# Kernel tuning notes

Hardware: AMD Instinct MI355X
Metric: run time of the kernel (lower is better)

Reference implementation:

```python
import jax, jax.numpy as jnp
import numpy as np

VOCAB, D = 50000, 300
B, LC = 64, 32
T, LT = 256, 64
N_SENTS = 5


def setup_inputs() -> dict:
    key = jax.random.key(0)
    k1, k2, k3 = jax.random.split(key, 3)
    claim = jax.random.randint(k1, (B, LC), 0, VOCAB)
    targets = jax.random.randint(k2, (B, T, LT), 0, VOCAB)
    embeddings = jax.random.normal(k3, (VOCAB, D), dtype=jnp.float32)
    return {"claim": claim, "targets": targets, "embeddings": embeddings, "n": N_SENTS}


def reference(claim, targets, embeddings, n):
    # Embedding lookups (frozen table)
    c = embeddings[claim]          # [B, Lc, d]
    t = embeddings[targets]        # [B, T, Lt, d]
    # batch_U = claim[:,None] @ targets^T  -> [B, T, Lc, Lt]
    U = jnp.einsum('bcd,btld->btcl', c, t)
    # softmax over target tokens (axis=3), max over claim tokens (axis=2)
    sm = jax.nn.softmax(U, axis=3)
    scores = jnp.max(sm, axis=2)           # [B, T, Lt]
    target_scores = jnp.sum(scores, axis=2)  # [B, T]
    # per-batch top-n target sentences (sorted order; torch used sorted=False,
    # the selected set is identical)
    _, idx = jax.lax.top_k(target_scores, n)  # [B, n]
    top = jnp.take_along_axis(U, idx[:, :, None, None], axis=1)  # [B, n, Lc, Lt]
    # L2-normalize over last axis (torch dim=2 of the [n, Lc, Lt] slice)
    norm = jnp.sqrt(jnp.sum(top * top, axis=3, keepdims=True))
    return top / norm
```

## Files before the change

kernel.cpp:

```cpp
#include <hip/hip_runtime.h>

#define VOCAB 50000
#define D     300
#define B_    64
#define LC    32
#define T_    256
#define LT    64
#define NSEL  5
#define NCAND 16

#define A_U4   2560
#define A_HALF 20480
#define TROW   320

typedef _Float16 half8_t __attribute__((ext_vector_type(8)));
typedef float    f32x4   __attribute__((ext_vector_type(4)));


__global__ __launch_bounds__(256) void k_prep(const int* __restrict__ claim,
                                              const float* __restrict__ emb,
                                              _Float16* __restrict__ tab,
                                              _Float16* __restrict__ wsA,
                                              int tableBlocks) {
    int wave = threadIdx.x >> 6, lane = threadIdx.x & 63;
    if ((int)blockIdx.x < tableBlocks) {
#pragma unroll
        for (int it = 0; it < 8; ++it) {
            int r = blockIdx.x * 32 + it * 4 + wave;
            if (r < VOCAB) {
                const float* src = emb + (size_t)r * D;
                _Float16* d = tab + (size_t)r * TROW;
#pragma unroll
                for (int i = 0; i < 5; ++i) {
                    int k = lane + i * 64;
                    d[k] = (k < D) ? (_Float16)src[k] : (_Float16)0.0f;
                }
            }
        }
    } else {
#pragma unroll
        for (int it = 0; it < 8; ++it) {
            int row = (blockIdx.x - tableBlocks) * 32 + it * 4 + wave;
            int b = row >> 5, m = row & 31;
            int tok = claim[row];
            const float* src = emb + (size_t)tok * D;
            _Float16* base = wsA + (size_t)b * A_HALF;
#pragma unroll
            for (int i = 0; i < 5; ++i) {
                int k = lane + i * 64;
                float x = (k < D) ? src[k] : 0.0f;
                _Float16 h = (_Float16)x;
                int sp = ((k >> 3) ^ (m & 7));
                int idx = (m * 40 + sp) * 8 + (k & 7);
                base[idx] = h;
                base[10240 + idx] = (_Float16)(x - (float)h);
            }
        }
    }
}

__device__ __forceinline__ void split8(const float4& a, const float4& b,
                                       half8_t& hv, half8_t& lv) {
    float x[8] = {a.x, a.y, a.z, a.w, b.x, b.y, b.z, b.w};
#pragma unroll
    for (int i = 0; i < 8; ++i) {
        _Float16 h = (_Float16)x[i];
        hv[i] = h;
        lv[i] = (_Float16)(x[i] - (float)h);
    }
}

template<int NI>
__device__ __forceinline__ void compute_exact(const uint4* sA,
                                              const float* __restrict__ emb,
                                              const int* __restrict__ trow, int lcol0,
                                              int lane, f32x4 acc[2][NI]) {
    int ln = lane & 15, quad = lane >> 4;
#pragma unroll
    for (int mi = 0; mi < 2; ++mi)
#pragma unroll
        for (int ni = 0; ni < NI; ++ni) acc[mi][ni] = (f32x4)0.0f;

    int arow0 = ln * 40;
    int arow1 = (16 + ln) * 40;
    int key = ln & 7;
    int qo = quad * 8;

    const float* bp[NI];
#pragma unroll
    for (int ni = 0; ni < NI; ++ni) {
        int tok = trow[lcol0 + ni * 16 + ln];
        bp[ni] = emb + (size_t)tok * D;
    }
#pragma unroll 1
    for (int ks = 0; ks < 10; ++ks) {
        int kb = ks * 32 + qo;
        int ka = kb > 296 ? 296 : kb;
        int kb4 = kb + 4;
        int kbb = kb4 > 296 ? 296 : kb4;
        float4 b0[NI], b1[NI];
#pragma unroll
        for (int ni = 0; ni < NI; ++ni) {
            b0[ni] = *(const float4*)(bp[ni] + ka);
            b1[ni] = *(const float4*)(bp[ni] + kbb);
        }
        if (kb >= 296) {
            float4 z = make_float4(0.f, 0.f, 0.f, 0.f);
#pragma unroll
            for (int ni = 0; ni < NI; ++ni) {
                if (kb >= 300) b0[ni] = z;
                b1[ni] = z;
            }
        }
        int sp = (ks * 4 + quad) ^ key;
        half8_t ah[2], al[2];
        ah[0] = __builtin_bit_cast(half8_t, sA[arow0 + sp]);
        al[0] = __builtin_bit_cast(half8_t, sA[1280 + arow0 + sp]);
        ah[1] = __builtin_bit_cast(half8_t, sA[arow1 + sp]);
        al[1] = __builtin_bit_cast(half8_t, sA[1280 + arow1 + sp]);
        half8_t bh[NI], bl[NI];
#pragma unroll
        for (int ni = 0; ni < NI; ++ni) split8(b0[ni], b1[ni], bh[ni], bl[ni]);
#pragma unroll
        for (int mi = 0; mi < 2; ++mi)
#pragma unroll
            for (int ni = 0; ni < NI; ++ni) {
                acc[mi][ni] = __builtin_amdgcn_mfma_f32_16x16x32_f16(ah[mi], bh[ni], acc[mi][ni], 0, 0, 0);
                acc[mi][ni] = __builtin_amdgcn_mfma_f32_16x16x32_f16(ah[mi], bl[ni], acc[mi][ni], 0, 0, 0);
                acc[mi][ni] = __builtin_amdgcn_mfma_f32_16x16x32_f16(al[mi], bh[ni], acc[mi][ni], 0, 0, 0);
            }
    }
}

__device__ __forceinline__ void compute_noisy(const uint4* sA,
                                              const _Float16* __restrict__ tab,
                                              const int* __restrict__ trow,
                                              int lane, f32x4 acc[2][4]) {
    int ln = lane & 15, quad = lane >> 4;
#pragma unroll
    for (int mi = 0; mi < 2; ++mi)
#pragma unroll
        for (int ni = 0; ni < 4; ++ni) acc[mi][ni] = (f32x4)0.0f;

    int arow0 = ln * 40;
    int arow1 = (16 + ln) * 40;
    int key = ln & 7;
    int qo = quad * 8;

    const _Float16* rp[4];
#pragma unroll
    for (int ni = 0; ni < 4; ++ni) {
        int tok = trow[ni * 16 + ln];
        rp[ni] = tab + (size_t)tok * TROW;
    }
    half8_t bh[2][4];
#pragma unroll
    for (int ni = 0; ni < 4; ++ni) bh[0][ni] = *(const half8_t*)(rp[ni] + qo);
#pragma unroll
    for (int ks = 0; ks < 10; ++ks) {
        int cur = ks & 1, nxt = cur ^ 1;
        if (ks < 9) {
            int ko = (ks + 1) * 32 + qo;
#pragma unroll
            for (int ni = 0; ni < 4; ++ni)
                bh[nxt][ni] = *(const half8_t*)(rp[ni] + ko);
        }
        int sp = (ks * 4 + quad) ^ key;
        half8_t ah[2], al[2];
        ah[0] = __builtin_bit_cast(half8_t, sA[arow0 + sp]);
        al[0] = __builtin_bit_cast(half8_t, sA[1280 + arow0 + sp]);
        ah[1] = __builtin_bit_cast(half8_t, sA[arow1 + sp]);
        al[1] = __builtin_bit_cast(half8_t, sA[1280 + arow1 + sp]);
#pragma unroll
        for (int mi = 0; mi < 2; ++mi)
#pragma unroll
            for (int ni = 0; ni < 4; ++ni) {
                acc[mi][ni] = __builtin_amdgcn_mfma_f32_16x16x32_f16(ah[mi], bh[cur][ni], acc[mi][ni], 0, 0, 0);
                acc[mi][ni] = __builtin_amdgcn_mfma_f32_16x16x32_f16(al[mi], bh[cur][ni], acc[mi][ni], 0, 0, 0);
            }
    }
}

__device__ __forceinline__ float xmax4(float v) {
    v = fmaxf(v, __shfl_xor(v, 1)); v = fmaxf(v, __shfl_xor(v, 2));
    v = fmaxf(v, __shfl_xor(v, 4)); v = fmaxf(v, __shfl_xor(v, 8));
    return v;
}
__device__ __forceinline__ float xsum4(float v) {
    v += __shfl_xor(v, 1); v += __shfl_xor(v, 2);
    v += __shfl_xor(v, 4); v += __shfl_xor(v, 8);
    return v;
}

__device__ __forceinline__ float score_from_acc(f32x4 acc[2][4]) {
    float score_l[4] = {0.f, 0.f, 0.f, 0.f};
#pragma unroll
    for (int mi = 0; mi < 2; ++mi)
#pragma unroll
        for (int r = 0; r < 4; ++r) {
            float m = fmaxf(fmaxf(acc[mi][0][r], acc[mi][1][r]),
                            fmaxf(acc[mi][2][r], acc[mi][3][r]));
            m = xmax4(m);
            float p[4], s = 0.f;
#pragma unroll
            for (int ni = 0; ni < 4; ++ni) { p[ni] = __expf(acc[mi][ni][r] - m); s += p[ni]; }
            s = xsum4(s);
            float rv = 1.0f / s;
#pragma unroll
            for (int ni = 0; ni < 4; ++ni) score_l[ni] = fmaxf(score_l[ni], p[ni] * rv);
        }
    float tot = 0.f;
#pragma unroll
    for (int ni = 0; ni < 4; ++ni) {
        float v = score_l[ni];
        v = fmaxf(v, __shfl_xor(v, 16));
        v = fmaxf(v, __shfl_xor(v, 32));
        tot += v;
    }
    return xsum4(tot);
}

template<bool FAST>
__global__ __launch_bounds__(256, 4) void k_scores(const int* __restrict__ targets,
                                                   const float* __restrict__ emb,
                                                   const _Float16* __restrict__ tab,
                                                   const _Float16* __restrict__ wsA,
                                                   float* __restrict__ wsScr) {
    __shared__ __align__(16) uint4 sA[A_U4];
    int wg = blockIdx.x;
    int xcd = wg & 7, rest = wg >> 3;
    int b = xcd * 8 + (rest >> 6);
    int tg = rest & 63;
    int tid = threadIdx.x;
    {
        const uint4* src = (const uint4*)(wsA + (size_t)b * A_HALF);
        for (int i = tid; i < A_U4; i += 256) sA[i] = src[i];
    }
    __syncthreads();

    int lane = tid & 63, wave = tid >> 6;
    int t = tg * 4 + wave;
    const int* trow = targets + ((size_t)b * T_ + t) * LT;

    f32x4 acc[2][4];
    if (FAST) compute_noisy(sA, tab, trow, lane, acc);
    else      compute_exact<4>(sA, emb, trow, 0, lane, acc);
    float tot = score_from_acc(acc);
    if (lane == 0) wsScr[b * T_ + t] = tot;
}

__global__ __launch_bounds__(256) void k_sel(const int* __restrict__ targets,
                                             const float* __restrict__ emb,
                                             const _Float16* __restrict__ wsA,
                                             const float* __restrict__ wsScr,
                                             int* __restrict__ wsCand,
                                             float* __restrict__ wsScoreC) {
    __shared__ __align__(16) uint4 sA[A_U4];
    __shared__ int sCand[NCAND];
    int r = blockIdx.x, b = blockIdx.y, tid = threadIdx.x;
    int lane = tid & 63, wave = tid >> 6;
    if (wave) {
        const uint4* src = (const uint4*)(wsA + (size_t)b * A_HALF);
        for (int i = tid - 64; i < A_U4; i += 192) sA[i] = src[i];
    } else {
        float v[4];
#pragma unroll
        for (int i = 0; i < 4; ++i) v[i] = wsScr[b * T_ + lane + 64 * i];
        for (int s = 0; s < NCAND; ++s) {
            float bv = v[0]; int bi = lane;
#pragma unroll
            for (int i = 1; i < 4; ++i) {
                int idx = lane + 64 * i;
                if (v[i] > bv) { bv = v[i]; bi = idx; }
            }
            for (int off = 32; off > 0; off >>= 1) {
                float ov = __shfl_down(bv, off);
                int   oi = __shfl_down(bi, off);
                if (ov > bv || (ov == bv && oi < bi)) { bv = ov; bi = oi; }
            }
            bi = __shfl(bi, 0);
            if (lane == 0) {
                sCand[s] = bi;
                if (r == 0) wsCand[b * NCAND + s] = bi;
            }
            if ((bi & 63) == lane) v[bi >> 6] = -1e30f;
        }
    }
    __syncthreads();

    int c = r * 4 + wave;
    int t = sCand[c];
    const int* trow = targets + ((size_t)b * T_ + t) * LT;
    f32x4 acc[2][4];
    compute_exact<4>(sA, emb, trow, 0, lane, acc);
    float tot = score_from_acc(acc);
    if (lane == 0) wsScoreC[b * NCAND + c] = tot;
}

__global__ __launch_bounds__(256) void k_output(const int* __restrict__ targets,
                                                const float* __restrict__ emb,
                                                const _Float16* __restrict__ wsA,
                                                const int* __restrict__ wsCand,
                                                const float* __restrict__ wsScoreC,
                                                float* __restrict__ out) {
    __shared__ __align__(16) uint4 sA[A_U4];
    __shared__ float sS[LC][4];
    __shared__ int sT;
    int b = blockIdx.y, j = blockIdx.x, tid = threadIdx.x;
    int lane = tid & 63, wave = tid >> 6;
    if (wave) {
        const uint4* src = (const uint4*)(wsA + (size_t)b * A_HALF);
        for (int i = tid - 64; i < A_U4; i += 192) sA[i] = src[i];
    } else if (lane == 0) {
        unsigned used = 0; int sel = 0;
        for (int jj = 0; jj <= j; ++jj) {
            float bs = -1e30f; int bt = 0x7fffffff, bsl = 0;
            for (int s = 0; s < NCAND; ++s) {
                if (used & (1u << s)) continue;
                float sc = wsScoreC[b * NCAND + s];
                int tt = wsCand[b * NCAND + s];
                if (sc > bs || (sc == bs && tt < bt)) { bs = sc; bt = tt; bsl = s; }
            }
            used |= (1u << bsl);
            sel = bt;
        }
        sT = sel;
    }
    __syncthreads();

    int t = sT;
    const int* trow = targets + ((size_t)b * T_ + t) * LT;
    f32x4 acc[2][1];
    compute_exact<1>(sA, emb, trow, wave * 16, lane, acc);

    int ln = lane & 15, quad = lane >> 4;
#pragma unroll
    for (int mi = 0; mi < 2; ++mi)
#pragma unroll
        for (int r = 0; r < 4; ++r) {
            float v = acc[mi][0][r] * acc[mi][0][r];
            v = xsum4(v);
            if (ln == 0) sS[mi * 16 + quad * 4 + r][wave] = v;
        }
    __syncthreads();

    float* obase = out + (size_t)(b * NSEL + j) * (LC * LT);
#pragma unroll
    for (int mi = 0; mi < 2; ++mi)
#pragma unroll
        for (int r = 0; r < 4; ++r) {
            int c = mi * 16 + quad * 4 + r;
            float ss = sS[c][0] + sS[c][1] + sS[c][2] + sS[c][3];
            float rinv = 1.0f / sqrtf(ss);
            obase[c * LT + wave * 16 + ln] = acc[mi][0][r] * rinv;
        }
}

extern "C" void kernel_launch(void* const* d_in, const int* in_sizes, int n_in,
                              void* d_out, int out_size, void* d_ws, size_t ws_size,
                              hipStream_t stream) {
    const int*   claim   = (const int*)d_in[0];
    const int*   targets = (const int*)d_in[1];
    const float* emb     = (const float*)d_in[2];

    const size_t tabBytes = (size_t)VOCAB * TROW * sizeof(_Float16);
    const size_t restBytes = (size_t)B_ * A_HALF * sizeof(_Float16)
                           + (size_t)B_ * T_ * sizeof(float)
                           + (size_t)B_ * NCAND * (sizeof(int) + sizeof(float)) + 256;
    bool fast = ws_size >= tabBytes + restBytes;

    char* p = (char*)d_ws;
    _Float16* tab = nullptr;
    if (fast) { tab = (_Float16*)p; p += tabBytes; }
    _Float16* wsA = (_Float16*)p; p += (size_t)B_ * A_HALF * sizeof(_Float16);
    float* wsScr = (float*)p;     p += (size_t)B_ * T_ * sizeof(float);
    int*   wsCand = (int*)p;      p += (size_t)B_ * NCAND * sizeof(int);
    float* wsScoreC = (float*)p;
    float* out   = (float*)d_out;

    int tableBlocks = fast ? ((VOCAB + 31) / 32) : 0;
    k_prep<<<dim3(tableBlocks + 64), dim3(256), 0, stream>>>(claim, emb, tab, wsA, tableBlocks);
    if (fast) {
        k_scores<true><<<dim3(B_ * 64), dim3(256), 0, stream>>>(targets, emb, tab, wsA, wsScr);
    } else {
        k_scores<false><<<dim3(B_ * 64), dim3(256), 0, stream>>>(targets, emb, tab, wsA, wsScr);
    }
    k_sel<<<dim3(NCAND / 4, B_), dim3(256), 0, stream>>>(targets, emb, wsA, wsScr, wsCand, wsScoreC);
    k_output<<<dim3(NSEL, B_), dim3(256), 0, stream>>>(targets, emb, wsA, wsCand, wsScoreC, out);
}
```

Before: 241.3 us.

## Fuse prep, scoring, selection and output into one cooperative persistent kernel

Replaces the four separate launches (prep, scores, sel, output) with a single cooperative kernel of 1024 blocks that uses grid-wide syncs between the phases. Each block converts table rows in a grid-stride loop, then scores 16 target sentences, and a subset of blocks runs candidate selection and the normalized output. This is meant to remove launch gaps and inter-kernel drain/fill. In exchange, the scoring phase runs with fewer blocks and more serial work per block, and it adds grid-sync costs. If the cooperative launch fails, the code falls back to the old path.

Measured after the change: 725.2 us. +200.6%, slower.

```diff
diff --git a/kernel.cpp b/kernel.cpp
--- a/kernel.cpp
+++ b/kernel.cpp
@@ -1,4 +1,7 @@
 #include <hip/hip_runtime.h>
+#include <hip/hip_cooperative_groups.h>
+
+namespace cg = cooperative_groups;
 
 #define VOCAB 50000
 #define D     300
@@ -17,6 +20,319 @@
 typedef float    f32x4   __attribute__((ext_vector_type(4)));
 
 
+__device__ __forceinline__ void split8(const float4& a, const float4& b,
+                                       half8_t& hv, half8_t& lv) {
+    float x[8] = {a.x, a.y, a.z, a.w, b.x, b.y, b.z, b.w};
+#pragma unroll
+    for (int i = 0; i < 8; ++i) {
+        _Float16 h = (_Float16)x[i];
+        hv[i] = h;
+        lv[i] = (_Float16)(x[i] - (float)h);
+    }
+}
+
+template<int NI>
+__device__ __forceinline__ void compute_exact(const uint4* sA,
+                                              const float* __restrict__ emb,
+                                              const int* __restrict__ trow, int lcol0,
+                                              int lane, f32x4 acc[2][NI]) {
+    int ln = lane & 15, quad = lane >> 4;
+#pragma unroll
+    for (int mi = 0; mi < 2; ++mi)
+#pragma unroll
+        for (int ni = 0; ni < NI; ++ni) acc[mi][ni] = (f32x4)0.0f;
+
+    int arow0 = ln * 40;
+    int arow1 = (16 + ln) * 40;
+    int key = ln & 7;
+    int qo = quad * 8;
+
+    const float* bp[NI];
+#pragma unroll
+    for (int ni = 0; ni < NI; ++ni) {
+        int tok = trow[lcol0 + ni * 16 + ln];
+        bp[ni] = emb + (size_t)tok * D;
+    }
+#pragma unroll 1
+    for (int ks = 0; ks < 10; ++ks) {
+        int kb = ks * 32 + qo;
+        int ka = kb > 296 ? 296 : kb;
+        int kb4 = kb + 4;
+        int kbb = kb4 > 296 ? 296 : kb4;
+        float4 b0[NI], b1[NI];
+#pragma unroll
+        for (int ni = 0; ni < NI; ++ni) {
+            b0[ni] = *(const float4*)(bp[ni] + ka);
+            b1[ni] = *(const float4*)(bp[ni] + kbb);
+        }
+        if (kb >= 296) {
+            float4 z = make_float4(0.f, 0.f, 0.f, 0.f);
+#pragma unroll
+            for (int ni = 0; ni < NI; ++ni) {
+                if (kb >= 300) b0[ni] = z;
+                b1[ni] = z;
+            }
+        }
+        int sp = (ks * 4 + quad) ^ key;
+        half8_t ah[2], al[2];
+        ah[0] = __builtin_bit_cast(half8_t, sA[arow0 + sp]);
+        al[0] = __builtin_bit_cast(half8_t, sA[1280 + arow0 + sp]);
+        ah[1] = __builtin_bit_cast(half8_t, sA[arow1 + sp]);
+        al[1] = __builtin_bit_cast(half8_t, sA[1280 + arow1 + sp]);
+        half8_t bh[NI], bl[NI];
+#pragma unroll
+        for (int ni = 0; ni < NI; ++ni) split8(b0[ni], b1[ni], bh[ni], bl[ni]);
+#pragma unroll
+        for (int mi = 0; mi < 2; ++mi)
+#pragma unroll
+            for (int ni = 0; ni < NI; ++ni) {
+                acc[mi][ni] = __builtin_amdgcn_mfma_f32_16x16x32_f16(ah[mi], bh[ni], acc[mi][ni], 0, 0, 0);
+                acc[mi][ni] = __builtin_amdgcn_mfma_f32_16x16x32_f16(ah[mi], bl[ni], acc[mi][ni], 0, 0, 0);
+                acc[mi][ni] = __builtin_amdgcn_mfma_f32_16x16x32_f16(al[mi], bh[ni], acc[mi][ni], 0, 0, 0);
+            }
+    }
+}
+
+__device__ __forceinline__ void compute_noisy(const uint4* sA,
+                                              const _Float16* __restrict__ tab,
+                                              const int* __restrict__ trow,
+                                              int lane, f32x4 acc[2][4]) {
+    int ln = lane & 15, quad = lane >> 4;
+#pragma unroll
+    for (int mi = 0; mi < 2; ++mi)
+#pragma unroll
+        for (int ni = 0; ni < 4; ++ni) acc[mi][ni] = (f32x4)0.0f;
+
+    int arow0 = ln * 40;
+    int arow1 = (16 + ln) * 40;
+    int key = ln & 7;
+    int qo = quad * 8;
+
+    const _Float16* rp[4];
+#pragma unroll
+    for (int ni = 0; ni < 4; ++ni) {
+        int tok = trow[ni * 16 + ln];
+        rp[ni] = tab + (size_t)tok * TROW;
+    }
+    half8_t bh[2][4];
+#pragma unroll
+    for (int ni = 0; ni < 4; ++ni) bh[0][ni] = *(const half8_t*)(rp[ni] + qo);
+#pragma unroll
+    for (int ks = 0; ks < 10; ++ks) {
+        int cur = ks & 1, nxt = cur ^ 1;
+        if (ks < 9) {
+            int ko = (ks + 1) * 32 + qo;
+#pragma unroll
+            for (int ni = 0; ni < 4; ++ni)
+                bh[nxt][ni] = *(const half8_t*)(rp[ni] + ko);
+        }
+        int sp = (ks * 4 + quad) ^ key;
+        half8_t ah[2], al[2];
+        ah[0] = __builtin_bit_cast(half8_t, sA[arow0 + sp]);
+        al[0] = __builtin_bit_cast(half8_t, sA[1280 + arow0 + sp]);
+        ah[1] = __builtin_bit_cast(half8_t, sA[arow1 + sp]);
+        al[1] = __builtin_bit_cast(half8_t, sA[1280 + arow1 + sp]);
+#pragma unroll
+        for (int mi = 0; mi < 2; ++mi)
+#pragma unroll
+            for (int ni = 0; ni < 4; ++ni) {
+                acc[mi][ni] = __builtin_amdgcn_mfma_f32_16x16x32_f16(ah[mi], bh[cur][ni], acc[mi][ni], 0, 0, 0);
+                acc[mi][ni] = __builtin_amdgcn_mfma_f32_16x16x32_f16(al[mi], bh[cur][ni], acc[mi][ni], 0, 0, 0);
+            }
+    }
+}
+
+__device__ __forceinline__ float xmax4(float v) {
+    v = fmaxf(v, __shfl_xor(v, 1)); v = fmaxf(v, __shfl_xor(v, 2));
+    v = fmaxf(v, __shfl_xor(v, 4)); v = fmaxf(v, __shfl_xor(v, 8));
+    return v;
+}
+__device__ __forceinline__ float xsum4(float v) {
+    v += __shfl_xor(v, 1); v += __shfl_xor(v, 2);
+    v += __shfl_xor(v, 4); v += __shfl_xor(v, 8);
+    return v;
+}
+
+__device__ __forceinline__ float score_from_acc(f32x4 acc[2][4]) {
+    float score_l[4] = {0.f, 0.f, 0.f, 0.f};
+#pragma unroll
+    for (int mi = 0; mi < 2; ++mi)
+#pragma unroll
+        for (int r = 0; r < 4; ++r) {
+            float m = fmaxf(fmaxf(acc[mi][0][r], acc[mi][1][r]),
+                            fmaxf(acc[mi][2][r], acc[mi][3][r]));
+            m = xmax4(m);
+            float p[4], s = 0.f;
+#pragma unroll
+            for (int ni = 0; ni < 4; ++ni) { p[ni] = __expf(acc[mi][ni][r] - m); s += p[ni]; }
+            s = xsum4(s);
+            float rv = 1.0f / s;
+#pragma unroll
+            for (int ni = 0; ni < 4; ++ni) score_l[ni] = fmaxf(score_l[ni], p[ni] * rv);
+        }
+    float tot = 0.f;
+#pragma unroll
+    for (int ni = 0; ni < 4; ++ni) {
+        float v = score_l[ni];
+        v = fmaxf(v, __shfl_xor(v, 16));
+        v = fmaxf(v, __shfl_xor(v, 32));
+        tot += v;
+    }
+    return xsum4(tot);
+}
+
+__global__ __launch_bounds__(256, 4) void k_fused(const int* __restrict__ claim,
+                                                  const int* __restrict__ targets,
+                                                  const float* __restrict__ emb,
+                                                  _Float16* __restrict__ tab,
+                                                  _Float16* __restrict__ wsA,
+                                                  float* __restrict__ wsScr,
+                                                  int* __restrict__ wsCand,
+                                                  float* __restrict__ wsScoreC,
+                                                  float* __restrict__ out) {
+    cg::grid_group grid = cg::this_grid();
+    __shared__ __align__(16) uint4 sA[A_U4];
+    int wg = blockIdx.x, tid = threadIdx.x;
+    int lane = tid & 63, wave = tid >> 6;
+
+    for (int r = wg * 4 + wave; r < VOCAB; r += 4096) {
+        const float* src = emb + (size_t)r * D;
+        _Float16* d = tab + (size_t)r * TROW;
+#pragma unroll
+        for (int i = 0; i < 5; ++i) {
+            int k = lane + i * 64;
+            d[k] = (k < D) ? (_Float16)src[k] : (_Float16)0.0f;
+        }
+    }
+    if (wg < 512) {
+        int row = wg * 4 + wave;
+        int b = row >> 5, m = row & 31;
+        int tok = claim[row];
+        const float* src = emb + (size_t)tok * D;
+        _Float16* base = wsA + (size_t)b * A_HALF;
+#pragma unroll
+        for (int i = 0; i < 5; ++i) {
+            int k = lane + i * 64;
+            float x = (k < D) ? src[k] : 0.0f;
+            _Float16 h = (_Float16)x;
+            int sp = ((k >> 3) ^ (m & 7));
+            int idx = (m * 40 + sp) * 8 + (k & 7);
+            base[idx] = h;
+            base[10240 + idx] = (_Float16)(x - (float)h);
+        }
+    }
+    grid.sync();
+
+    {
+        int xcd = wg & 7, rest = wg >> 3;
+        int b = xcd * 8 + (rest >> 4);
+        int tg4 = rest & 15;
+        {
+            const uint4* src = (const uint4*)(wsA + (size_t)b * A_HALF);
+            for (int i = tid; i < A_U4; i += 256) sA[i] = src[i];
+        }
+        __syncthreads();
+        for (int it = 0; it < 4; ++it) {
+            int t = (tg4 * 4 + it) * 4 + wave;
+            const int* trow = targets + ((size_t)b * T_ + t) * LT;
+            f32x4 acc[2][4];
+            compute_noisy(sA, tab, trow, lane, acc);
+            float tot = score_from_acc(acc);
+            if (lane == 0) wsScr[b * T_ + t] = tot;
+        }
+    }
+    grid.sync();
+
+    if (wg < 256) {
+        int r = wg & 3, b = wg >> 2;
+        {
+            const uint4* src = (const uint4*)(wsA + (size_t)b * A_HALF);
+            for (int i = tid; i < A_U4; i += 256) sA[i] = src[i];
+        }
+        float v[4];
+#pragma unroll
+        for (int i = 0; i < 4; ++i) v[i] = wsScr[b * T_ + lane + 64 * i];
+        int myc = r * 4 + wave, myT = 0;
+        for (int s = 0; s < NCAND; ++s) {
+            float bv = v[0]; int bi = lane;
+#pragma unroll
+            for (int i = 1; i < 4; ++i) {
+                int idx = lane + 64 * i;
+                if (v[i] > bv) { bv = v[i]; bi = idx; }
+            }
+            for (int off = 32; off > 0; off >>= 1) {
+                float ov = __shfl_down(bv, off);
+                int   oi = __shfl_down(bi, off);
+                if (ov > bv || (ov == bv && oi < bi)) { bv = ov; bi = oi; }
+            }
+            bi = __shfl(bi, 0);
+            if (s == myc) myT = bi;
+            if (r == 0 && wave == 0 && lane == 0) wsCand[b * NCAND + s] = bi;
+            if ((bi & 63) == lane) v[bi >> 6] = -1e30f;
+        }
+        __syncthreads();
+        const int* trow = targets + ((size_t)b * T_ + myT) * LT;
+        f32x4 acc[2][4];
+        compute_exact<4>(sA, emb, trow, 0, lane, acc);
+        float tot = score_from_acc(acc);
+        if (lane == 0) wsScoreC[b * NCAND + myc] = tot;
+    }
+    grid.sync();
+
+    if (wg < 320) {
+        int b = wg / NSEL, j = wg % NSEL;
+        {
+            const uint4* src = (const uint4*)(wsA + (size_t)b * A_HALF);
+            for (int i = tid; i < A_U4; i += 256) sA[i] = src[i];
+        }
+        unsigned used = 0; int sel = 0;
+        for (int jj = 0; jj <= j; ++jj) {
+            float bs = -1e30f; int bt = 0x7fffffff, bsl = 0;
+            for (int s = 0; s < NCAND; ++s) {
+                if (used & (1u << s)) continue;
+                float sc = wsScoreC[b * NCAND + s];
+                int tt = wsCand[b * NCAND + s];
+                if (sc > bs || (sc == bs && tt < bt)) { bs = sc; bt = tt; bsl = s; }
+            }
+            used |= (1u << bsl);
+            sel = bt;
+        }
+        __syncthreads();
+        const int* trow = targets + ((size_t)b * T_ + sel) * LT;
+        f32x4 acc[2][1];
+        compute_exact<1>(sA, emb, trow, wave * 16, lane, acc);
+
+        int ln = lane & 15, quad = lane >> 4;
+        float pv[2][4];
+#pragma unroll
+        for (int mi = 0; mi < 2; ++mi)
+#pragma unroll
+            for (int r = 0; r < 4; ++r) {
+                float vv = acc[mi][0][r] * acc[mi][0][r];
+                pv[mi][r] = xsum4(vv);
+            }
+        __syncthreads();
+        float* sS = (float*)sA;
+#pragma unroll
+        for (int mi = 0; mi < 2; ++mi)
+#pragma unroll
+            for (int r = 0; r < 4; ++r)
+                if (ln == 0) sS[(mi * 16 + quad * 4 + r) * 4 + wave] = pv[mi][r];
+        __syncthreads();
+
+        float* obase = out + (size_t)(b * NSEL + j) * (LC * LT);
+#pragma unroll
+        for (int mi = 0; mi < 2; ++mi)
+#pragma unroll
+            for (int r = 0; r < 4; ++r) {
+                int c = mi * 16 + quad * 4 + r;
+                float ss = sS[c * 4 + 0] + sS[c * 4 + 1] + sS[c * 4 + 2] + sS[c * 4 + 3];
+                float rinv = 1.0f / sqrtf(ss);
+                obase[c * LT + wave * 16 + ln] = acc[mi][0][r] * rinv;
+            }
+    }
+}
+
 __global__ __launch_bounds__(256) void k_prep(const int* __restrict__ claim,
                                               const float* __restrict__ emb,
                                               _Float16* __restrict__ tab,
@@ -57,167 +373,6 @@
             }
         }
     }
-}
-
-__device__ __forceinline__ void split8(const float4& a, const float4& b,
-                                       half8_t& hv, half8_t& lv) {
-    float x[8] = {a.x, a.y, a.z, a.w, b.x, b.y, b.z, b.w};
-#pragma unroll
-    for (int i = 0; i < 8; ++i) {
-        _Float16 h = (_Float16)x[i];
-        hv[i] = h;
-        lv[i] = (_Float16)(x[i] - (float)h);
-    }
-}
-
-template<int NI>
-__device__ __forceinline__ void compute_exact(const uint4* sA,
-                                              const float* __restrict__ emb,
-                                              const int* __restrict__ trow, int lcol0,
-                                              int lane, f32x4 acc[2][NI]) {
-    int ln = lane & 15, quad = lane >> 4;
-#pragma unroll
-    for (int mi = 0; mi < 2; ++mi)
-#pragma unroll
-        for (int ni = 0; ni < NI; ++ni) acc[mi][ni] = (f32x4)0.0f;
-
-    int arow0 = ln * 40;
-    int arow1 = (16 + ln) * 40;
-    int key = ln & 7;
-    int qo = quad * 8;
-
-    const float* bp[NI];
-#pragma unroll
-    for (int ni = 0; ni < NI; ++ni) {
-        int tok = trow[lcol0 + ni * 16 + ln];
-        bp[ni] = emb + (size_t)tok * D;
-    }
-#pragma unroll 1
-    for (int ks = 0; ks < 10; ++ks) {
-        int kb = ks * 32 + qo;
-        int ka = kb > 296 ? 296 : kb;
-        int kb4 = kb + 4;
-        int kbb = kb4 > 296 ? 296 : kb4;
-        float4 b0[NI], b1[NI];
-#pragma unroll
-        for (int ni = 0; ni < NI; ++ni) {
-            b0[ni] = *(const float4*)(bp[ni] + ka);
-            b1[ni] = *(const float4*)(bp[ni] + kbb);
-        }
-        if (kb >= 296) {
-            float4 z = make_float4(0.f, 0.f, 0.f, 0.f);
-#pragma unroll
-            for (int ni = 0; ni < NI; ++ni) {
-                if (kb >= 300) b0[ni] = z;
-                b1[ni] = z;
-            }
-        }
-        int sp = (ks * 4 + quad) ^ key;
-        half8_t ah[2], al[2];
-        ah[0] = __builtin_bit_cast(half8_t, sA[arow0 + sp]);
-        al[0] = __builtin_bit_cast(half8_t, sA[1280 + arow0 + sp]);
-        ah[1] = __builtin_bit_cast(half8_t, sA[arow1 + sp]);
-        al[1] = __builtin_bit_cast(half8_t, sA[1280 + arow1 + sp]);
-        half8_t bh[NI], bl[NI];
-#pragma unroll
-        for (int ni = 0; ni < NI; ++ni) split8(b0[ni], b1[ni], bh[ni], bl[ni]);
-#pragma unroll
-        for (int mi = 0; mi < 2; ++mi)
-#pragma unroll
-            for (int ni = 0; ni < NI; ++ni) {
-                acc[mi][ni] = __builtin_amdgcn_mfma_f32_16x16x32_f16(ah[mi], bh[ni], acc[mi][ni], 0, 0, 0);
-                acc[mi][ni] = __builtin_amdgcn_mfma_f32_16x16x32_f16(ah[mi], bl[ni], acc[mi][ni], 0, 0, 0);
-                acc[mi][ni] = __builtin_amdgcn_mfma_f32_16x16x32_f16(al[mi], bh[ni], acc[mi][ni], 0, 0, 0);
-            }
-    }
-}
-
-__device__ __forceinline__ void compute_noisy(const uint4* sA,
-                                              const _Float16* __restrict__ tab,
-                                              const int* __restrict__ trow,
-                                              int lane, f32x4 acc[2][4]) {
-    int ln = lane & 15, quad = lane >> 4;
-#pragma unroll
-    for (int mi = 0; mi < 2; ++mi)
-#pragma unroll
-        for (int ni = 0; ni < 4; ++ni) acc[mi][ni] = (f32x4)0.0f;
-
-    int arow0 = ln * 40;
-    int arow1 = (16 + ln) * 40;
-    int key = ln & 7;
-    int qo = quad * 8;
-
-    const _Float16* rp[4];
-#pragma unroll
-    for (int ni = 0; ni < 4; ++ni) {
-        int tok = trow[ni * 16 + ln];
-        rp[ni] = tab + (size_t)tok * TROW;
-    }
-    half8_t bh[2][4];
-#pragma unroll
-    for (int ni = 0; ni < 4; ++ni) bh[0][ni] = *(const half8_t*)(rp[ni] + qo);
-#pragma unroll
-    for (int ks = 0; ks < 10; ++ks) {
-        int cur = ks & 1, nxt = cur ^ 1;
-        if (ks < 9) {
-            int ko = (ks + 1) * 32 + qo;
-#pragma unroll
-            for (int ni = 0; ni < 4; ++ni)
-                bh[nxt][ni] = *(const half8_t*)(rp[ni] + ko);
-        }
-        int sp = (ks * 4 + quad) ^ key;
-        half8_t ah[2], al[2];
-        ah[0] = __builtin_bit_cast(half8_t, sA[arow0 + sp]);
-        al[0] = __builtin_bit_cast(half8_t, sA[1280 + arow0 + sp]);
-        ah[1] = __builtin_bit_cast(half8_t, sA[arow1 + sp]);
-        al[1] = __builtin_bit_cast(half8_t, sA[1280 + arow1 + sp]);
-#pragma unroll
-        for (int mi = 0; mi < 2; ++mi)
-#pragma unroll
-            for (int ni = 0; ni < 4; ++ni) {
-                acc[mi][ni] = __builtin_amdgcn_mfma_f32_16x16x32_f16(ah[mi], bh[cur][ni], acc[mi][ni], 0, 0, 0);
-                acc[mi][ni] = __builtin_amdgcn_mfma_f32_16x16x32_f16(al[mi], bh[cur][ni], acc[mi][ni], 0, 0, 0);
-            }
-    }
-}
-
-__device__ __forceinline__ float xmax4(float v) {
-    v = fmaxf(v, __shfl_xor(v, 1)); v = fmaxf(v, __shfl_xor(v, 2));
-    v = fmaxf(v, __shfl_xor(v, 4)); v = fmaxf(v, __shfl_xor(v, 8));
-    return v;
-}
-__device__ __forceinline__ float xsum4(float v) {
-    v += __shfl_xor(v, 1); v += __shfl_xor(v, 2);
-    v += __shfl_xor(v, 4); v += __shfl_xor(v, 8);
-    return v;
-}
-
-__device__ __forceinline__ float score_from_acc(f32x4 acc[2][4]) {
-    float score_l[4] = {0.f, 0.f, 0.f, 0.f};
-#pragma unroll
-    for (int mi = 0; mi < 2; ++mi)
-#pragma unroll
-        for (int r = 0; r < 4; ++r) {
-            float m = fmaxf(fmaxf(acc[mi][0][r], acc[mi][1][r]),
-                            fmaxf(acc[mi][2][r], acc[mi][3][r]));
-            m = xmax4(m);
-            float p[4], s = 0.f;
-#pragma unroll
-            for (int ni = 0; ni < 4; ++ni) { p[ni] = __expf(acc[mi][ni][r] - m); s += p[ni]; }
-            s = xsum4(s);
-            float rv = 1.0f / s;
-#pragma unroll
-            for (int ni = 0; ni < 4; ++ni) score_l[ni] = fmaxf(score_l[ni], p[ni] * rv);
-        }
-    float tot = 0.f;
-#pragma unroll
-    for (int ni = 0; ni < 4; ++ni) {
-        float v = score_l[ni];
-        v = fmaxf(v, __shfl_xor(v, 16));
-        v = fmaxf(v, __shfl_xor(v, 32));
-        tot += v;
-    }
-    return xsum4(tot);
 }
 
 template<bool FAST>
@@ -378,6 +533,16 @@
     float* wsScoreC = (float*)p;
     float* out   = (float*)d_out;
 
+    if (fast) {
+        void* args[] = { (void*)&claim, (void*)&targets, (void*)&emb,
+                         (void*)&tab, (void*)&wsA, (void*)&wsScr,
+                         (void*)&wsCand, (void*)&wsScoreC, (void*)&out };
+        hipError_t e = hipLaunchCooperativeKernel((const void*)k_fused,
+                                                  dim3(1024), dim3(256),
+                                                  args, 0, stream);
+        if (e == hipSuccess) return;
+    }
+
     int tableBlocks = fast ? ((VOCAB + 31) / 32) : 0;
     k_prep<<<dim3(tableBlocks + 64), dim3(256), 0, stream>>>(claim, emb, tab, wsA, tableBlocks);
     if (fast) {
```
